# Kernel optimization log

Measured on AMD Instinct MI355X. Metric: run time of the kernel, lower is better.

Reference implementation:

```python
import jax, jax.numpy as jnp
import numpy as np

N = 10000
E = 160000
H = 8
C = 128
D = 1024
NB = 3
NG = 64
NEG_SLOPE = 0.2
BN_EPS = 1e-5


def setup_inputs() -> dict:
    key = jax.random.key(0)
    ks = jax.random.split(key, 12)
    x = jax.random.normal(ks[0], (N, D), dtype=jnp.float32)
    edge_index = jax.random.randint(ks[1], (2, E), 0, N, dtype=jnp.int64)
    batch = jnp.sort(jax.random.randint(ks[2], (N,), 0, NG, dtype=jnp.int64))
    W = jax.random.normal(ks[3], (NB, D, D), dtype=jnp.float32) * 0.03
    att_src = jax.random.normal(ks[4], (NB, H, C), dtype=jnp.float32) * 0.1
    att_dst = jax.random.normal(ks[5], (NB, H, C), dtype=jnp.float32) * 0.1
    att_bias = jnp.zeros((NB, D), dtype=jnp.float32)
    gamma = jnp.ones((NB, D), dtype=jnp.float32)
    beta = jnp.zeros((NB, D), dtype=jnp.float32)
    W_out = jax.random.normal(ks[6], (D, 2), dtype=jnp.float32) * 0.03
    b_out = jnp.zeros((2,), dtype=jnp.float32)
    return {"x": x, "edge_index": edge_index, "batch": batch, "W": W,
            "att_src": att_src, "att_dst": att_dst, "att_bias": att_bias,
            "gamma": gamma, "beta": beta, "W_out": W_out, "b_out": b_out}


def _gat_conv(x, Wb, a_src, a_dst, bias, src, dst):
    # linear projection, per-head view: [N, H, C]
    h = (x @ Wb).reshape(N, H, C)
    alpha_src = jnp.einsum('nhc,hc->nh', h, a_src)  # [N,H]
    alpha_dst = jnp.einsum('nhc,hc->nh', h, a_dst)
    e = jax.nn.leaky_relu(alpha_src[src] + alpha_dst[dst], NEG_SLOPE)  # [Etot,H]
    # segment softmax over incoming edges per destination node
    m = jax.ops.segment_max(e, dst, num_segments=N)  # every node has self-loop
    ex = jnp.exp(e - m[dst])
    denom = jax.ops.segment_sum(ex, dst, num_segments=N)
    alpha = ex / denom[dst]  # [Etot,H]
    msg = alpha[:, :, None] * h[src]  # [Etot,H,C]
    out = jax.ops.segment_sum(msg, dst, num_segments=N).reshape(N, H * C)
    return out + bias


def _batchnorm(x, g, b):
    mu = jnp.mean(x, axis=0)
    var = jnp.mean(jnp.square(x - mu), axis=0)  # biased, training mode
    return (x - mu) * jax.lax.rsqrt(var + BN_EPS) * g + b


def reference(x, edge_index, batch, W, att_src, att_dst, att_bias, gamma, beta, W_out, b_out):
    # add self loops (PyG GATConv default)
    loop = jnp.arange(N, dtype=edge_index.dtype)
    src = jnp.concatenate([edge_index[0], loop])
    dst = jnp.concatenate([edge_index[1], loop])

    h = x
    prev = x
    for i in range(NB):
        att = _gat_conv(h, W[i], att_src[i], att_dst[i], att_bias[i], src, dst)
        o = jax.nn.relu(_batchnorm(prev + att, gamma[i], beta[i]))
        prev = h
        h = o

    # global mean pool over graphs
    sums = jax.ops.segment_sum(h, batch, num_segments=NG)
    cnts = jax.ops.segment_sum(jnp.ones((N,), dtype=h.dtype), batch, num_segments=NG)
    pooled = sums / jnp.maximum(cnts, 1.0)[:, None]
    return pooled @ W_out + b_out
```

## Files before the change

kernel.cpp:

```cpp
#include <hip/hip_runtime.h>
#include <hip/hip_bf16.h>

#define N_NODES 10000
#define E_EDGES 160000
#define ETOT    170000
#define H_HEADS 8
#define C_CH    128
#define D_DIM   1024
#define NBLK    3
#define NGRAPH  64
#define NEG_SLOPE 0.2f
#define BN_EPS  1e-5f

typedef __attribute__((ext_vector_type(8))) _Float16 half8;
typedef __attribute__((ext_vector_type(4))) _Float16 half4;
typedef __attribute__((ext_vector_type(2))) _Float16 half2v;
typedef __attribute__((ext_vector_type(4))) float f32x4;

__device__ inline int lower_bound_batch(const int* __restrict__ batch, int g) {
    int lo = 0, hi = N_NODES;
    while (lo < hi) {
        int mid = (lo + hi) >> 1;
        if (batch[mid] < g) lo = mid + 1;
        else hi = mid;
    }
    return lo;
}

__global__ void deg_kernel(const int* __restrict__ ei, int* __restrict__ deg) {
    int tid = blockIdx.x * blockDim.x + threadIdx.x;
    if (tid >= ETOT) return;
    int dst = (tid < E_EDGES) ? ei[E_EDGES + tid] : (tid - E_EDGES);
    atomicAdd(&deg[dst], 1);
}

__global__ void scan_kernel(const int* __restrict__ deg, int* __restrict__ ioff) {
    __shared__ int part[256];
    int t = threadIdx.x;
    const int CH = (N_NODES + 255) / 256;
    int base = t * CH;
    int s = 0;
    for (int j = 0; j < CH; ++j) {
        int idx = base + j;
        if (idx < N_NODES) s += deg[idx];
    }
    part[t] = s;
    __syncthreads();
    for (int o = 1; o < 256; o <<= 1) {
        int v = 0;
        if (t >= o) v = part[t - o];
        __syncthreads();
        part[t] += v;
        __syncthreads();
    }
    int run = (t == 0) ? 0 : part[t - 1];
    for (int j = 0; j < CH; ++j) {
        int idx = base + j;
        if (idx < N_NODES) { ioff[idx] = run; run += deg[idx]; }
    }
}

__global__ void scatter_kernel(const int* __restrict__ ei, int* __restrict__ ioff,
                               int* __restrict__ csr_src, int* __restrict__ csr_dst) {
    int tid = blockIdx.x * blockDim.x + threadIdx.x;
    if (tid >= ETOT) return;
    int src, dst;
    if (tid < E_EDGES) { src = ei[tid]; dst = ei[E_EDGES + tid]; }
    else { src = dst = tid - E_EDGES; }
    int pos = atomicAdd(&ioff[dst], 1);
    csr_src[pos] = src;
    csr_dst[pos] = dst;
}

__global__ __launch_bounds__(256) void xconv_kernel(const float* __restrict__ in,
                                                    _Float16* __restrict__ o, int n4) {
    int i = blockIdx.x * blockDim.x + threadIdx.x;
    if (i >= n4) return;
    float4 v = ((const float4*)in)[i];
    half4 h = {(_Float16)v.x, (_Float16)v.y, (_Float16)v.z, (_Float16)v.w};
    ((half4*)o)[i] = h;
}

__global__ __launch_bounds__(256) void wtconv_kernel(const float* __restrict__ Wall,
                                                     _Float16* __restrict__ t16all) {
    const float* W = Wall + (size_t)blockIdx.z * D_DIM * D_DIM;
    _Float16* t16 = t16all + (size_t)blockIdx.z * D_DIM * D_DIM;
    __shared__ float t[32][33];
    int bn = blockIdx.x * 32;
    int bk = blockIdx.y * 32;
    int tx = threadIdx.x & 31;
    int ty = threadIdx.x >> 5;
#pragma unroll
    for (int r = 0; r < 32; r += 8)
        t[ty + r][tx] = W[(size_t)(bk + ty + r) * D_DIM + bn + tx];
    __syncthreads();
#pragma unroll
    for (int r = 0; r < 32; r += 8)
        t16[(size_t)(bn + ty + r) * D_DIM + bk + tx] = (_Float16)t[tx][ty + r];
}

__global__ __launch_bounds__(256) void gemm_mfma_kernel(const _Float16* __restrict__ A,
                                                        const _Float16* __restrict__ Bt,
                                                        _Float16* __restrict__ Hout,
                                                        const float* __restrict__ att_s,
                                                        const float* __restrict__ att_d,
                                                        float* __restrict__ asrc,
                                                        float* __restrict__ adst,
                                                        float* __restrict__ stats, int M) {
    __shared__ short As[128 * 32];
    __shared__ short Bs[128 * 32];
    __shared__ float sA[128], sD[128];
    int bx = blockIdx.x;
    int tid = threadIdx.x;
    if (bx == 0) {
#pragma unroll
        for (int j = 0; j < 8; ++j) stats[tid + j * 256] = 0.f;
    }
    int c = bx & 7;
    int head = (bx >> 3) & 7;
    int mt = c + 8 * (bx >> 6);
    if (mt >= 79) return;
    int bm = mt * 128;
    int bn = head * 128;
    int wave = tid >> 6;
    int lane = tid & 63;
    int wm = (wave >> 1) * 64;
    int wn = (wave & 1) * 64;
    int quad = lane >> 4;
    int l16 = lane & 15;

    f32x4 acc[4][4];
#pragma unroll
    for (int i = 0; i < 4; ++i)
#pragma unroll
        for (int j = 0; j < 4; ++j) acc[i][j] = (f32x4){0.f, 0.f, 0.f, 0.f};

    int srow = lane >> 2;
    int scol = (lane & 3) * 16;

    for (int kb = 0; kb < 32; ++kb) {
        int k0 = kb * 32;
#pragma unroll
        for (int r = 0; r < 2; ++r) {
            int arow = wave * 16 + r * 64 + srow;
            int grow = bm + arow;
            if (grow > M - 1) grow = M - 1;
            const char* gp = (const char*)(A + (size_t)grow * 1024 + k0) + scol;
            __builtin_amdgcn_global_load_lds(
                (const __attribute__((address_space(1))) void*)gp,
                (__attribute__((address_space(3))) void*)((char*)As + (wave * 16 + r * 64) * 64),
                16, 0, 0);
        }
#pragma unroll
        for (int r = 0; r < 2; ++r) {
            int brow = wave * 16 + r * 64 + srow;
            const char* gp = (const char*)(Bt + (size_t)(bn + brow) * 1024 + k0) + scol;
            __builtin_amdgcn_global_load_lds(
                (const __attribute__((address_space(1))) void*)gp,
                (__attribute__((address_space(3))) void*)((char*)Bs + (wave * 16 + r * 64) * 64),
                16, 0, 0);
        }
        __syncthreads();

        half8 af[4], bfr[4];
#pragma unroll
        for (int i = 0; i < 4; ++i)
            af[i] = *(const half8*)(As + (wm + i * 16 + l16) * 32 + quad * 8);
#pragma unroll
        for (int j = 0; j < 4; ++j)
            bfr[j] = *(const half8*)(Bs + (wn + j * 16 + l16) * 32 + quad * 8);
#pragma unroll
        for (int i = 0; i < 4; ++i)
#pragma unroll
            for (int j = 0; j < 4; ++j)
                acc[i][j] = __builtin_amdgcn_mfma_f32_16x16x32_f16(af[i], bfr[j], acc[i][j], 0, 0, 0);
        __syncthreads();
    }

    float wsv[4], wdv[4];
#pragma unroll
    for (int j = 0; j < 4; ++j) {
        int cc = wn + j * 16 + l16;
        wsv[j] = att_s[head * 128 + cc];
        wdv[j] = att_d[head * 128 + cc];
    }
    float psv[4][4], pdv[4][4];
#pragma unroll
    for (int i = 0; i < 4; ++i) {
#pragma unroll
        for (int reg = 0; reg < 4; ++reg) {
            float p = acc[i][0][reg] * wsv[0] + acc[i][1][reg] * wsv[1] +
                      acc[i][2][reg] * wsv[2] + acc[i][3][reg] * wsv[3];
            float q = acc[i][0][reg] * wdv[0] + acc[i][1][reg] * wdv[1] +
                      acc[i][2][reg] * wdv[2] + acc[i][3][reg] * wdv[3];
#pragma unroll
            for (int o = 1; o < 16; o <<= 1) {
                p += __shfl_xor(p, o);
                q += __shfl_xor(q, o);
            }
            psv[i][reg] = p;
            pdv[i][reg] = q;
        }
    }
    if ((wave & 1) == 0 && l16 == 0) {
#pragma unroll
        for (int i = 0; i < 4; ++i)
#pragma unroll
            for (int reg = 0; reg < 4; ++reg) {
                int r = wm + i * 16 + quad * 4 + reg;
                sA[r] = psv[i][reg];
                sD[r] = pdv[i][reg];
            }
    }
#pragma unroll
    for (int i = 0; i < 4; ++i) {
#pragma unroll
        for (int reg = 0; reg < 4; ++reg) {
            int gr = bm + wm + i * 16 + quad * 4 + reg;
            if (gr < M) {
                _Float16* hp = Hout + (size_t)head * N_NODES * 128 + (size_t)gr * 128 + wn + l16;
#pragma unroll
                for (int j = 0; j < 4; ++j) hp[j * 16] = (_Float16)acc[i][j][reg];
            }
        }
    }
    __syncthreads();
    if ((wave & 1) == 1 && l16 == 0) {
#pragma unroll
        for (int i = 0; i < 4; ++i)
#pragma unroll
            for (int reg = 0; reg < 4; ++reg) {
                int r = wm + i * 16 + quad * 4 + reg;
                int gr = bm + r;
                if (gr < M) {
                    asrc[gr * 8 + head] = sA[r] + psv[i][reg];
                    adst[gr * 8 + head] = sD[r] + pdv[i][reg];
                }
            }
    }
}

__global__ __launch_bounds__(256) void edge_exp_kernel(const int* __restrict__ csr_src,
                                                       const int* __restrict__ csr_dst,
                                                       const float* __restrict__ asrc,
                                                       const float* __restrict__ adst,
                                                       float* __restrict__ exw) {
    int p = blockIdx.x * 256 + threadIdx.x;
    if (p >= ETOT) return;
    int s = csr_src[p];
    int d = csr_dst[p];
    float4 s0 = *(const float4*)(asrc + (unsigned)s * 8u);
    float4 s1 = *(const float4*)(asrc + (unsigned)s * 8u + 4u);
    float4 d0 = *(const float4*)(adst + (unsigned)d * 8u);
    float4 d1 = *(const float4*)(adst + (unsigned)d * 8u + 4u);
    float e[8] = {s0.x + d0.x, s0.y + d0.y, s0.z + d0.z, s0.w + d0.w,
                  s1.x + d1.x, s1.y + d1.y, s1.z + d1.z, s1.w + d1.w};
    float4 o0, o1;
#pragma unroll
    for (int j = 0; j < 8; ++j) {
        float v = e[j];
        v = (v > 0.f) ? v : NEG_SLOPE * v;
        float ex = __expf(v);
        if (j < 4) ((float*)&o0)[j] = ex;
        else ((float*)&o1)[j - 4] = ex;
    }
    *(float4*)(exw + (unsigned)p * 8u) = o0;
    *(float4*)(exw + (unsigned)p * 8u + 4u) = o1;
}

__global__ __launch_bounds__(256) void agg_kernel(const _Float16* __restrict__ h16,
                                                  const float* __restrict__ exw,
                                                  const int* __restrict__ ioff,
                                                  const int* __restrict__ csr_src,
                                                  const _Float16* __restrict__ prevh,
                                                  const float* __restrict__ bias,
                                                  _Float16* __restrict__ yout) {
    int bx = blockIdx.x;
    int tid = threadIdx.x;
    int head = bx & 7;
    int chunk = bx >> 3;
    int sub = tid >> 5;
    int lane = tid & 31;
    int n = chunk * 8 + sub;
    unsigned c4 = (unsigned)(lane * 4);
    const _Float16* hh = h16 + (size_t)head * N_NODES * 128;
    const float* exh = exw + head;
    int start = (n == 0) ? 0 : ioff[n - 1];
    int end = ioff[n];
    float den = 0.f;
    float4 acc = make_float4(0.f, 0.f, 0.f, 0.f);
    int p = start;
    for (; p + 4 <= end; p += 4) {
        int s0 = csr_src[p + 0];
        int s1 = csr_src[p + 1];
        int s2 = csr_src[p + 2];
        int s3 = csr_src[p + 3];
        float x0 = exh[(unsigned)p * 8u];
        float x1 = exh[(unsigned)p * 8u + 8u];
        float x2 = exh[(unsigned)p * 8u + 16u];
        float x3 = exh[(unsigned)p * 8u + 24u];
        half4 h0 = *(const half4*)(hh + ((unsigned)s0 * 128u + c4));
        half4 h1 = *(const half4*)(hh + ((unsigned)s1 * 128u + c4));
        half4 h2 = *(const half4*)(hh + ((unsigned)s2 * 128u + c4));
        half4 h3 = *(const half4*)(hh + ((unsigned)s3 * 128u + c4));
        den += (x0 + x1) + (x2 + x3);
        acc.x = fmaf(x0, (float)h0[0], fmaf(x1, (float)h1[0], fmaf(x2, (float)h2[0], fmaf(x3, (float)h3[0], acc.x))));
        acc.y = fmaf(x0, (float)h0[1], fmaf(x1, (float)h1[1], fmaf(x2, (float)h2[1], fmaf(x3, (float)h3[1], acc.y))));
        acc.z = fmaf(x0, (float)h0[2], fmaf(x1, (float)h1[2], fmaf(x2, (float)h2[2], fmaf(x3, (float)h3[2], acc.z))));
        acc.w = fmaf(x0, (float)h0[3], fmaf(x1, (float)h1[3], fmaf(x2, (float)h2[3], fmaf(x3, (float)h3[3], acc.w))));
    }
    for (; p < end; ++p) {
        int s = csr_src[p];
        float x = exh[(unsigned)p * 8u];
        half4 hv = *(const half4*)(hh + ((unsigned)s * 128u + c4));
        den += x;
        acc.x = fmaf(x, (float)hv[0], acc.x);
        acc.y = fmaf(x, (float)hv[1], acc.y);
        acc.z = fmaf(x, (float)hv[2], acc.z);
        acc.w = fmaf(x, (float)hv[3], acc.w);
    }
    float invd = 1.0f / den;
    int col = head * 128 + (int)c4;
    half4 ph = *(const half4*)(prevh + (size_t)n * 1024 + col);
    float4 bv = *(const float4*)(bias + col);
    float r0 = fmaf(acc.x, invd, (float)ph[0] + bv.x);
    float r1 = fmaf(acc.y, invd, (float)ph[1] + bv.y);
    float r2 = fmaf(acc.z, invd, (float)ph[2] + bv.z);
    float r3 = fmaf(acc.w, invd, (float)ph[3] + bv.w);
    half4 o = {(_Float16)r0, (_Float16)r1, (_Float16)r2, (_Float16)r3};
    *(half4*)(yout + (size_t)n * 1024 + col) = o;
}

__global__ void bn_stats_kernel(const _Float16* __restrict__ y, float* __restrict__ stats) {
    int col = (blockIdx.x * 256 + threadIdx.x) * 2;
    float s0 = 0.f, s1 = 0.f, q0 = 0.f, q1 = 0.f;
    for (int r = blockIdx.y; r < N_NODES; r += gridDim.y) {
        half2v v = *(const half2v*)(y + (size_t)r * 1024 + col);
        float a = (float)v[0], b = (float)v[1];
        s0 += a; q0 += a * a;
        s1 += b; q1 += b * b;
    }
    atomicAdd(&stats[col], s0);
    atomicAdd(&stats[col + 1], s1);
    atomicAdd(&stats[1024 + col], q0);
    atomicAdd(&stats[1024 + col + 1], q1);
}

__global__ void bn_apply_kernel(const _Float16* __restrict__ y, const float* __restrict__ stats,
                                const float* __restrict__ gamma, const float* __restrict__ beta,
                                _Float16* __restrict__ oout) {
    int idx4 = blockIdx.x * blockDim.x + threadIdx.x;
    if (idx4 >= N_NODES * D_DIM / 4) return;
    int base = idx4 * 4;
    int col = base & 1023;
    const float invN = 1.0f / (float)N_NODES;
    half4 v = ((const half4*)y)[idx4];
    float r[4];
#pragma unroll
    for (int j = 0; j < 4; ++j) {
        int cc = col + j;
        float mu = stats[cc] * invN;
        float var = stats[1024 + cc] * invN - mu * mu;
        float t = ((float)v[j] - mu) * rsqrtf(var + BN_EPS) * gamma[cc] + beta[cc];
        r[j] = fmaxf(t, 0.f);
    }
    half4 h = {(_Float16)r[0], (_Float16)r[1], (_Float16)r[2], (_Float16)r[3]};
    ((half4*)oout)[idx4] = h;
}

__global__ __launch_bounds__(256) void pool_kernel(const _Float16* __restrict__ h3,
                                                   const int* __restrict__ batch,
                                                   float* __restrict__ pooled) {
    int g = blockIdx.y;
    int col = threadIdx.x * 4;
    int lo = lower_bound_batch(batch, g);
    int hi = lower_bound_batch(batch, g + 1);
    int len = hi - lo;
    int r0 = lo + (int)(((long long)len * blockIdx.x) >> 3);
    int r1 = lo + (int)(((long long)len * (blockIdx.x + 1)) >> 3);
    float a0 = 0.f, a1 = 0.f, a2 = 0.f, a3 = 0.f;
    for (int r = r0; r < r1; ++r) {
        half4 v = *(const half4*)(h3 + (size_t)r * 1024 + col);
        a0 += (float)v[0]; a1 += (float)v[1]; a2 += (float)v[2]; a3 += (float)v[3];
    }
    if (r1 > r0) {
        atomicAdd(&pooled[(size_t)g * 1024 + col + 0], a0);
        atomicAdd(&pooled[(size_t)g * 1024 + col + 1], a1);
        atomicAdd(&pooled[(size_t)g * 1024 + col + 2], a2);
        atomicAdd(&pooled[(size_t)g * 1024 + col + 3], a3);
    }
}

__global__ void final_kernel(const float* __restrict__ pooled, const int* __restrict__ batch,
                             const float* __restrict__ Wout, const float* __restrict__ bout,
                             float* __restrict__ out) {
    int g = blockIdx.x;
    int t = threadIdx.x;
    float p0 = 0.f, p1 = 0.f;
    for (int d = t; d < 1024; d += 256) {
        float v = pooled[(size_t)g * 1024 + d];
        p0 = fmaf(v, Wout[2 * d], p0);
        p1 = fmaf(v, Wout[2 * d + 1], p1);
    }
    __shared__ float s0[256], s1[256];
    s0[t] = p0; s1[t] = p1;
    __syncthreads();
    for (int o = 128; o; o >>= 1) {
        if (t < o) { s0[t] += s0[t + o]; s1[t] += s1[t + o]; }
        __syncthreads();
    }
    if (t == 0) {
        int cnt = lower_bound_batch(batch, g + 1) - lower_bound_batch(batch, g);
        float inv = 1.0f / fmaxf((float)cnt, 1.0f);
        out[g * 2 + 0] = s0[0] * inv + bout[0];
        out[g * 2 + 1] = s1[0] * inv + bout[1];
    }
}

extern "C" void kernel_launch(void* const* d_in, const int* in_sizes, int n_in,
                              void* d_out, int out_size, void* d_ws, size_t ws_size,
                              hipStream_t stream) {
    const float* x        = (const float*)d_in[0];
    const int*   ei       = (const int*)d_in[1];
    const int*   batch    = (const int*)d_in[2];
    const float* W        = (const float*)d_in[3];
    const float* att_src  = (const float*)d_in[4];
    const float* att_dst  = (const float*)d_in[5];
    const float* att_bias = (const float*)d_in[6];
    const float* gamma    = (const float*)d_in[7];
    const float* beta     = (const float*)d_in[8];
    const float* Wout     = (const float*)d_in[9];
    const float* bout     = (const float*)d_in[10];
    float* out = (float*)d_out;

    const size_t ND = (size_t)N_NODES * D_DIM;
    float* ws = (float*)d_ws;
    float* asrc   = ws;
    float* adst   = asrc + (size_t)N_NODES * H_HEADS;
    float* stats  = adst + (size_t)N_NODES * H_HEADS;
    float* pooled = stats + 2 * D_DIM;
    int* ideg     = (int*)(pooled + (size_t)NGRAPH * D_DIM);
    int* ioff     = ideg + N_NODES;
    int* csr_src  = ioff + N_NODES;
    int* csr_dst  = csr_src + ETOT;
    float* exw    = (float*)(csr_dst + ETOT);
    _Float16* bufP  = (_Float16*)(exw + (size_t)ETOT * H_HEADS);
    _Float16* bufO0 = bufP + ND;
    _Float16* h16   = bufO0 + ND;
    _Float16* y16   = h16 + ND;
    _Float16* Wt3   = y16 + ND;

    hipMemsetAsync(ideg, 0, N_NODES * sizeof(int), stream);
    hipMemsetAsync(pooled, 0, (size_t)NGRAPH * D_DIM * sizeof(float), stream);
    deg_kernel<<<(ETOT + 255) / 256, 256, 0, stream>>>(ei, ideg);
    scan_kernel<<<1, 256, 0, stream>>>(ideg, ioff);
    scatter_kernel<<<(ETOT + 255) / 256, 256, 0, stream>>>(ei, ioff, csr_src, csr_dst);
    xconv_kernel<<<(int)(ND / 4 + 255) / 256, 256, 0, stream>>>(x, bufP, (int)(ND / 4));
    wtconv_kernel<<<dim3(32, 32, 3), 256, 0, stream>>>(W, Wt3);

    const _Float16* Ain[3]  = {bufP, bufO0, bufP};
    const _Float16* Pin[3]  = {bufP, bufP, bufO0};
    _Float16* Oout[3]       = {bufO0, bufP, bufP};

    for (int i = 0; i < NBLK; ++i) {
        gemm_mfma_kernel<<<640, 256, 0, stream>>>(
            Ain[i], Wt3 + (size_t)i * D_DIM * D_DIM, h16,
            att_src + i * H_HEADS * C_CH, att_dst + i * H_HEADS * C_CH,
            asrc, adst, stats, N_NODES);
        edge_exp_kernel<<<(ETOT + 255) / 256, 256, 0, stream>>>(csr_src, csr_dst,
                                                                asrc, adst, exw);
        agg_kernel<<<N_NODES, 256, 0, stream>>>(h16, exw, ioff, csr_src,
                                                Pin[i], att_bias + i * D_DIM, y16);
        bn_stats_kernel<<<dim3(2, 128), 256, 0, stream>>>(y16, stats);
        bn_apply_kernel<<<(int)(ND / 4 + 255) / 256, 256, 0, stream>>>(
            y16, stats, gamma + i * D_DIM, beta + i * D_DIM, Oout[i]);
    }

    pool_kernel<<<dim3(8, NGRAPH), 256, 0, stream>>>(bufP, batch, pooled);
    final_kernel<<<NGRAPH, 256, 0, stream>>>(pooled, batch, Wout, bout, out);
}
```

Baseline: 585.5 us.

## Double-buffer GEMM LDS tiles and XOR-swizzle layout to avoid bank conflicts

The MFMA GEMM now keeps two LDS buffers for the A and B tiles and prefetches the next K-slice with global_load_lds while computing on the current one. This removes one barrier per iteration and is meant to overlap global loads with MFMA work. The LDS column slot is XOR-swizzled by row, both in the store addresses and in the fragment reads, to cut bank conflicts. LDS use doubles, which could lower occupancy.

```diff
diff --git a/kernel.cpp b/kernel.cpp
--- a/kernel.cpp
+++ b/kernel.cpp
@@ -107,8 +107,8 @@
                                                         float* __restrict__ asrc,
                                                         float* __restrict__ adst,
                                                         float* __restrict__ stats, int M) {
-    __shared__ short As[128 * 32];
-    __shared__ short Bs[128 * 32];
+    __shared__ short As[2 * 128 * 32];
+    __shared__ short Bs[2 * 128 * 32];
     __shared__ float sA[128], sD[128];
     int bx = blockIdx.x;
     int tid = threadIdx.x;
@@ -136,46 +136,67 @@
         for (int j = 0; j < 4; ++j) acc[i][j] = (f32x4){0.f, 0.f, 0.f, 0.f};
 
     int srow = lane >> 2;
-    int scol = (lane & 3) * 16;
-
+    int sslotb = (((lane & 3) ^ ((srow >> 1) & 3)) << 4);
+    int arow0 = wave * 16 + srow;
+    int arow1 = wave * 16 + 64 + srow;
+    int ga0 = bm + arow0; if (ga0 > M - 1) ga0 = M - 1;
+    int ga1 = bm + arow1; if (ga1 > M - 1) ga1 = M - 1;
+    const char* gA0 = (const char*)(A + (size_t)ga0 * 1024) + sslotb;
+    const char* gA1 = (const char*)(A + (size_t)ga1 * 1024) + sslotb;
+    const char* gB0 = (const char*)(Bt + (size_t)(bn + arow0) * 1024) + sslotb;
+    const char* gB1 = (const char*)(Bt + (size_t)(bn + arow1) * 1024) + sslotb;
+    char* lA0 = (char*)As + arow0 * 64 - srow * 64 + 0;
+    char* ldA0 = (char*)As + (wave * 16) * 64;
+    char* ldA1 = (char*)As + (wave * 16 + 64) * 64;
+    char* ldB0 = (char*)Bs + (wave * 16) * 64;
+    char* ldB1 = (char*)Bs + (wave * 16 + 64) * 64;
+    (void)lA0;
+
+#define STAGE(bufofs, kbyte)                                                          \
+    do {                                                                              \
+        __builtin_amdgcn_global_load_lds(                                             \
+            (const __attribute__((address_space(1))) void*)(gA0 + (kbyte)),           \
+            (__attribute__((address_space(3))) void*)(ldA0 + (bufofs)), 16, 0, 0);    \
+        __builtin_amdgcn_global_load_lds(                                             \
+            (const __attribute__((address_space(1))) void*)(gA1 + (kbyte)),           \
+            (__attribute__((address_space(3))) void*)(ldA1 + (bufofs)), 16, 0, 0);    \
+        __builtin_amdgcn_global_load_lds(                                             \
+            (const __attribute__((address_space(1))) void*)(gB0 + (kbyte)),           \
+            (__attribute__((address_space(3))) void*)(ldB0 + (bufofs)), 16, 0, 0);    \
+        __builtin_amdgcn_global_load_lds(                                             \
+            (const __attribute__((address_space(1))) void*)(gB1 + (kbyte)),           \
+            (__attribute__((address_space(3))) void*)(ldB1 + (bufofs)), 16, 0, 0);    \
+    } while (0)
+
+    STAGE(0, 0);
+    __syncthreads();
+
+    int rsw = (l16 >> 1) & 3;
+    int cur = 0;
     for (int kb = 0; kb < 32; ++kb) {
-        int k0 = kb * 32;
-#pragma unroll
-        for (int r = 0; r < 2; ++r) {
-            int arow = wave * 16 + r * 64 + srow;
-            int grow = bm + arow;
-            if (grow > M - 1) grow = M - 1;
-            const char* gp = (const char*)(A + (size_t)grow * 1024 + k0) + scol;
-            __builtin_amdgcn_global_load_lds(
-                (const __attribute__((address_space(1))) void*)gp,
-                (__attribute__((address_space(3))) void*)((char*)As + (wave * 16 + r * 64) * 64),
-                16, 0, 0);
+        if (kb < 31) {
+            int bo = (cur ^ 1) * 8192;
+            int kbyte = (kb + 1) * 64;
+            STAGE(bo, kbyte);
         }
-#pragma unroll
-        for (int r = 0; r < 2; ++r) {
-            int brow = wave * 16 + r * 64 + srow;
-            const char* gp = (const char*)(Bt + (size_t)(bn + brow) * 1024 + k0) + scol;
-            __builtin_amdgcn_global_load_lds(
-                (const __attribute__((address_space(1))) void*)gp,
-                (__attribute__((address_space(3))) void*)((char*)Bs + (wave * 16 + r * 64) * 64),
-                16, 0, 0);
-        }
-        __syncthreads();
-
+        const short* Ab = As + cur * 4096;
+        const short* Bb = Bs + cur * 4096;
         half8 af[4], bfr[4];
 #pragma unroll
         for (int i = 0; i < 4; ++i)
-            af[i] = *(const half8*)(As + (wm + i * 16 + l16) * 32 + quad * 8);
+            af[i] = *(const half8*)(Ab + (wm + i * 16 + l16) * 32 + ((quad ^ rsw) * 8));
 #pragma unroll
         for (int j = 0; j < 4; ++j)
-            bfr[j] = *(const half8*)(Bs + (wn + j * 16 + l16) * 32 + quad * 8);
+            bfr[j] = *(const half8*)(Bb + (wn + j * 16 + l16) * 32 + ((quad ^ rsw) * 8));
 #pragma unroll
         for (int i = 0; i < 4; ++i)
 #pragma unroll
             for (int j = 0; j < 4; ++j)
                 acc[i][j] = __builtin_amdgcn_mfma_f32_16x16x32_f16(af[i], bfr[j], acc[i][j], 0, 0, 0);
         __syncthreads();
-    }
+        cur ^= 1;
+    }
+#undef STAGE
 
     float wsv[4], wdv[4];
 #pragma unroll
```

Result: slower. 606.1 us (+3.5%).
